# Kernel tuning notes

Measured on AMD Instinct MI355X. Metric: run time of the kernel, lower is better.

The kernel has to match this reference:

```python
import jax, jax.numpy as jnp
import numpy as np
import math

SIZE = 64
SCALE = math.sqrt(SIZE)
EPS = 1e-12  # torch F.normalize default eps

def l2_normalize(x, axis):
    n = jnp.linalg.norm(x, ord=2, axis=axis, keepdims=True)
    return x / jnp.maximum(n, EPS)

def setup_inputs() -> dict:
    key = jax.random.key(0)
    k1, k2, k3 = jax.random.split(key, 3)
    n, l, s, d, v = 8, 2048, 2048, SIZE, SIZE
    return {
        "query": jax.random.normal(k1, (n, l, d), dtype=jnp.float32),
        "key": jax.random.normal(k2, (n, s, d), dtype=jnp.float32),
        "value": jax.random.normal(k3, (n, s, v), dtype=jnp.float32),
        "mask": jnp.ones((n, l, s), dtype=bool),
    }

def reference(query, key, value, mask):
    # rank-3 query path with normalize=True (cosine attention)
    q = l2_normalize(query, 2)
    k = l2_normalize(key, 2)
    score = jnp.einsum('nlk,nsk->nls', q, k) / SCALE
    score = jnp.where(mask, score, -jnp.inf)
    score = jax.nn.softmax(score, axis=2)  # [n, l, s]
    # equivalent to (score.unsqueeze(3) * value.unsqueeze(1)).sum(2)
    output_value = jnp.einsum('nls,nsv->nlv', score, value)
    return (output_value, score)
```

## Files before the change

kernel.cpp:

```cpp
#include <hip/hip_runtime.h>
#include <hip/hip_bf16.h>
#include <math.h>


typedef __bf16 bf16x8 __attribute__((ext_vector_type(8)));
typedef __bf16 bf16x4 __attribute__((ext_vector_type(4)));
typedef float f32x4 __attribute__((ext_vector_type(4)));

#define NB 8
#define LL 2048
#define SS 2048
#define DD 64

__global__ __launch_bounds__(256) void prep_norm(const float* __restrict__ q,
                                                 const float* __restrict__ k,
                                                 __bf16* __restrict__ Qb,
                                                 __bf16* __restrict__ Kb) {
  int w = threadIdx.x >> 6, lane = threadIdx.x & 63;
  int r = blockIdx.x * 4 + w;
  const float* src;
  __bf16* dst;
  float extra;
  if (r < NB * LL) {
    src = q + (size_t)r * DD;
    dst = Qb + (size_t)r * DD;
    extra = 0.125f;
  } else {
    int rk = r - NB * LL;
    src = k + (size_t)rk * DD;
    dst = Kb + (size_t)rk * DD;
    extra = 1.0f;
  }
  float x = src[lane];
  float ss = x * x;
  ss += __shfl_xor(ss, 1);
  ss += __shfl_xor(ss, 2);
  ss += __shfl_xor(ss, 4);
  ss += __shfl_xor(ss, 8);
  ss += __shfl_xor(ss, 16);
  ss += __shfl_xor(ss, 32);
  float nrm = sqrtf(ss);
  float sc = extra / fmaxf(nrm, 1e-12f);
  dst[lane] = (__bf16)(x * sc);
}

__global__ __launch_bounds__(256) void prep_vt(const float* __restrict__ v,
                                               __bf16* __restrict__ Vt) {
  __shared__ __bf16 tile[64][72];
  int n = blockIdx.y;
  int s0 = blockIdx.x * 64;
  int t = threadIdx.x;
#pragma unroll
  for (int it = 0; it < 4; ++it) {
    int idx = t + it * 256;
    int s = idx >> 4, c = idx & 15;
    float4 f = *(const float4*)(v + ((size_t)(n * SS + s0 + s)) * DD + c * 4);
    tile[s][c * 4 + 0] = (__bf16)f.x;
    tile[s][c * 4 + 1] = (__bf16)f.y;
    tile[s][c * 4 + 2] = (__bf16)f.z;
    tile[s][c * 4 + 3] = (__bf16)f.w;
  }
  __syncthreads();
#pragma unroll
  for (int it = 0; it < 4; ++it) {
    int idx = t + it * 256;
    int vv = idx >> 4, c = idx & 15;
    bf16x4 o;
    o[0] = tile[c * 4 + 0][vv];
    o[1] = tile[c * 4 + 1][vv];
    o[2] = tile[c * 4 + 2][vv];
    o[3] = tile[c * 4 + 3][vv];
    *(bf16x4*)(Vt + ((size_t)(n * DD + vv)) * SS + s0 + c * 4) = o;
  }
}

__global__ __launch_bounds__(512, 4) void attn_main(const __bf16* __restrict__ Qb,
                                                    const __bf16* __restrict__ Kb,
                                                    const __bf16* __restrict__ Vt,
                                                    const int* __restrict__ mask,
                                                    float* __restrict__ out_val,
                                                    float* __restrict__ out_score) {
  __shared__ __bf16 e_lds[2][16][136];
  __shared__ unsigned mb_lds[2][16][33];
  __shared__ float rs_lds[8][16];
  __shared__ float acc_red[4][16][17];
  __shared__ float inv_row[16];
  __shared__ __bf16 ep_buf[16][520];

  const int n = blockIdx.y;
  const int l0 = blockIdx.x * 16;

  const int t = threadIdx.x;
  const int w = t >> 6;
  const int lane = t & 63;
  const int m16 = lane & 15;
  const int quad = lane >> 4;
  const int vg = w & 3;
  const int sh = (w >> 2) * 64;

  const __bf16* qrow = Qb + ((size_t)(n * LL + l0 + m16)) * DD;
  bf16x8 aq0 = *(const bf16x8*)(qrow + quad * 8);
  bf16x8 aq1 = *(const bf16x8*)(qrow + 32 + quad * 8);

  const __bf16* kbase = Kb + (size_t)n * SS * DD;
  const __bf16* vrow = Vt + ((size_t)(n * DD + vg * 16 + m16)) * SS + sh;

  const int mrow_st = t >> 5;
  const int mcol_st = (t & 31) * 4;
  const int* mgbase = mask + ((size_t)(n * LL + l0 + mrow_st)) * SS + mcol_st;

  f32x4 acc_o = {0.f, 0.f, 0.f, 0.f};
  float rsum = 0.f;
  bf16x4 stash[16];

  int4 mreg[2];
  mreg[0] = *(const int4*)(mgbase + 0 * 128);
  mreg[1] = *(const int4*)(mgbase + 1 * 128);

  bf16x8 kpa0, kpa1, kpb0, kpb1;
  {
    const __bf16* kr = kbase + (size_t)(w * 16 + m16) * DD;
    kpa0 = *(const bf16x8*)(kr + quad * 8);
    kpa1 = *(const bf16x8*)(kr + 32 + quad * 8);
  }

  {
    const int4 m = mreg[0];
    mb_lds[0][mrow_st][t & 31] = (unsigned)((m.x != 0) | ((m.y != 0) << 8) |
                                            ((m.z != 0) << 16) | ((m.w != 0) << 24));
  }
  asm volatile("s_waitcnt lgkmcnt(0)" ::: "memory");
  __builtin_amdgcn_s_barrier();

#pragma unroll
  for (int c = 0; c < 16; ++c) {
    const int sc = c * 128;
    bf16x8 bv0 = *(const bf16x8*)(vrow + sc + quad * 8);
    bf16x8 bv1 = *(const bf16x8*)(vrow + sc + 32 + quad * 8);
    if (c + 1 < 16) {
      const __bf16* kr = kbase + (size_t)(sc + 128 + w * 16 + m16) * DD;
      if (c & 1) {
        kpa0 = *(const bf16x8*)(kr + quad * 8);
        kpa1 = *(const bf16x8*)(kr + 32 + quad * 8);
      } else {
        kpb0 = *(const bf16x8*)(kr + quad * 8);
        kpb1 = *(const bf16x8*)(kr + 32 + quad * 8);
      }
    }
    if (c + 2 < 16) mreg[c & 1] = *(const int4*)(mgbase + (size_t)(c + 2) * 128);
    if (c + 1 < 16) {
      const int4 m = mreg[(c + 1) & 1];
      mb_lds[(c + 1) & 1][mrow_st][t & 31] =
          (unsigned)((m.x != 0) | ((m.y != 0) << 8) | ((m.z != 0) << 16) |
                     ((m.w != 0) << 24));
    }
    const unsigned mu = mb_lds[c & 1][m16][w * 4 + quad];
    const bf16x8 kb0 = (c & 1) ? kpb0 : kpa0;
    const bf16x8 kb1 = (c & 1) ? kpb1 : kpa1;
    f32x4 acc = {0.f, 0.f, 0.f, 0.f};
    acc = __builtin_amdgcn_mfma_f32_16x16x32_bf16(kb0, aq0, acc, 0, 0, 0);
    acc = __builtin_amdgcn_mfma_f32_16x16x32_bf16(kb1, aq1, acc, 0, 0, 0);
    float e0 = (mu & 0x1u) ? __expf(acc[0]) : 0.f;
    float e1 = (mu & 0x100u) ? __expf(acc[1]) : 0.f;
    float e2 = (mu & 0x10000u) ? __expf(acc[2]) : 0.f;
    float e3 = (mu & 0x1000000u) ? __expf(acc[3]) : 0.f;
    rsum += (e0 + e1) + (e2 + e3);
    bf16x4 sv;
    sv[0] = (__bf16)e0;
    sv[1] = (__bf16)e1;
    sv[2] = (__bf16)e2;
    sv[3] = (__bf16)e3;
    stash[c] = sv;
    *(bf16x4*)(&e_lds[c & 1][m16][w * 16 + quad * 4]) = sv;
    asm volatile("s_waitcnt lgkmcnt(0)" ::: "memory");
    __builtin_amdgcn_s_barrier();
    bf16x8 ae0 = *(const bf16x8*)(&e_lds[c & 1][m16][sh + quad * 8]);
    bf16x8 ae1 = *(const bf16x8*)(&e_lds[c & 1][m16][sh + 32 + quad * 8]);
    acc_o = __builtin_amdgcn_mfma_f32_16x16x32_bf16(ae0, bv0, acc_o, 0, 0, 0);
    acc_o = __builtin_amdgcn_mfma_f32_16x16x32_bf16(ae1, bv1, acc_o, 0, 0, 0);
  }

  rsum += __shfl_xor(rsum, 16);
  rsum += __shfl_xor(rsum, 32);
  if (quad == 0) rs_lds[w][m16] = rsum;
  if (w >= 4) {
#pragma unroll
    for (int r = 0; r < 4; ++r) acc_red[vg][quad * 4 + r][m16] = acc_o[r];
  }
  __syncthreads();

  float tot = 0.f;
#pragma unroll
  for (int ww = 0; ww < 8; ++ww) tot += rs_lds[ww][m16];
  const float inv_s = 1.0f / tot;
  if (t < 16) inv_row[t] = inv_s;

  if (w < 4) {
#pragma unroll
    for (int r = 0; r < 4; ++r) {
      const int row = quad * 4 + r;
      float tr = 0.f;
#pragma unroll
      for (int ww = 0; ww < 8; ++ww) tr += rs_lds[ww][row];
      const float o = (acc_o[r] + acc_red[vg][row][m16]) / tr;
      out_val[((size_t)(n * LL + l0 + row)) * DD + vg * 16 + m16] = o;
    }
  }
  __syncthreads();

  const int erow = t >> 5;
  const int ecol = (t & 31) * 4;
  const float einv = inv_row[erow];
  float* obase = out_score + ((size_t)(n * LL + l0 + erow)) * SS;
#pragma unroll
  for (int g = 0; g < 4; ++g) {
#pragma unroll
    for (int i = 0; i < 4; ++i) {
      *(bf16x4*)(&ep_buf[m16][i * 128 + w * 16 + quad * 4]) = stash[g * 4 + i];
    }
    asm volatile("s_waitcnt lgkmcnt(0)" ::: "memory");
    __builtin_amdgcn_s_barrier();
#pragma unroll
    for (int i = 0; i < 4; ++i) {
      const bf16x4 ev = *(const bf16x4*)(&ep_buf[erow][ecol + i * 128]);
      float4 o;
      o.x = (float)ev[0] * einv;
      o.y = (float)ev[1] * einv;
      o.z = (float)ev[2] * einv;
      o.w = (float)ev[3] * einv;
      *(float4*)(obase + g * 512 + ecol + i * 128) = o;
    }
    asm volatile("s_waitcnt lgkmcnt(0)" ::: "memory");
    __builtin_amdgcn_s_barrier();
  }
}

extern "C" void kernel_launch(void* const* d_in, const int* in_sizes, int n_in,
                              void* d_out, int out_size, void* d_ws, size_t ws_size,
                              hipStream_t stream) {
  const float* q = (const float*)d_in[0];
  const float* k = (const float*)d_in[1];
  const float* v = (const float*)d_in[2];
  const int* mask = (const int*)d_in[3];

  float* out_val = (float*)d_out;
  float* out_score = out_val + (size_t)NB * LL * DD;

  __bf16* Qb = (__bf16*)d_ws;
  __bf16* Kb = Qb + (size_t)NB * LL * DD;
  __bf16* Vt = Kb + (size_t)NB * SS * DD;

  prep_norm<<<dim3((NB * LL * 2) / 4), dim3(256), 0, stream>>>(q, k, Qb, Kb);
  prep_vt<<<dim3(SS / 64, NB), dim3(256), 0, stream>>>(v, Vt);
  attn_main<<<dim3(LL / 16, NB), dim3(512), 0, stream>>>(Qb, Kb, Vt, mask, out_val, out_score);
}
```

Before: 278.1 us.

## Split attention into two passes: row sums first, then stream scores during PV

The main kernel now runs two passes over the keys. The first recomputes QK^T and exponentials only to get row sums, and caches the mask bits in registers. The second recomputes QK^T, does the PV MMA, and writes each normalized score tile straight out as it is produced. This removes the 16-entry register stash and the epilogue LDS buffer, and spreads the score stores across the loop so they overlap compute. The cost is a second set of K loads, MMAs and exps, plus extra barriers in the first pass.

```diff
diff --git a/kernel.cpp b/kernel.cpp
--- a/kernel.cpp
+++ b/kernel.cpp
@@ -85,7 +85,6 @@
   __shared__ float rs_lds[8][16];
   __shared__ float acc_red[4][16][17];
   __shared__ float inv_row[16];
-  __shared__ __bf16 ep_buf[16][520];
 
   const int n = blockIdx.y;
   const int l0 = blockIdx.x * 16;
@@ -103,26 +102,22 @@
   bf16x8 aq1 = *(const bf16x8*)(qrow + 32 + quad * 8);
 
   const __bf16* kbase = Kb + (size_t)n * SS * DD;
+  const __bf16* krow0 = kbase + (size_t)(w * 16 + m16) * DD;
   const __bf16* vrow = Vt + ((size_t)(n * DD + vg * 16 + m16)) * SS + sh;
 
   const int mrow_st = t >> 5;
-  const int mcol_st = (t & 31) * 4;
-  const int* mgbase = mask + ((size_t)(n * LL + l0 + mrow_st)) * SS + mcol_st;
-
-  f32x4 acc_o = {0.f, 0.f, 0.f, 0.f};
+  const int* mgbase = mask + ((size_t)(n * LL + l0 + mrow_st)) * SS + (t & 31) * 4;
+
   float rsum = 0.f;
-  bf16x4 stash[16];
+  unsigned mbits0 = 0, mbits1 = 0;
 
   int4 mreg[2];
   mreg[0] = *(const int4*)(mgbase + 0 * 128);
   mreg[1] = *(const int4*)(mgbase + 1 * 128);
 
   bf16x8 kpa0, kpa1, kpb0, kpb1;
-  {
-    const __bf16* kr = kbase + (size_t)(w * 16 + m16) * DD;
-    kpa0 = *(const bf16x8*)(kr + quad * 8);
-    kpa1 = *(const bf16x8*)(kr + 32 + quad * 8);
-  }
+  kpa0 = *(const bf16x8*)(krow0 + quad * 8);
+  kpa1 = *(const bf16x8*)(krow0 + 32 + quad * 8);
 
   {
     const int4 m = mreg[0];
@@ -134,11 +129,8 @@
 
 #pragma unroll
   for (int c = 0; c < 16; ++c) {
-    const int sc = c * 128;
-    bf16x8 bv0 = *(const bf16x8*)(vrow + sc + quad * 8);
-    bf16x8 bv1 = *(const bf16x8*)(vrow + sc + 32 + quad * 8);
     if (c + 1 < 16) {
-      const __bf16* kr = kbase + (size_t)(sc + 128 + w * 16 + m16) * DD;
+      const __bf16* kr = krow0 + (size_t)((c + 1) * 128) * DD;
       if (c & 1) {
         kpa0 = *(const bf16x8*)(kr + quad * 8);
         kpa1 = *(const bf16x8*)(kr + 32 + quad * 8);
@@ -160,17 +152,75 @@
     f32x4 acc = {0.f, 0.f, 0.f, 0.f};
     acc = __builtin_amdgcn_mfma_f32_16x16x32_bf16(kb0, aq0, acc, 0, 0, 0);
     acc = __builtin_amdgcn_mfma_f32_16x16x32_bf16(kb1, aq1, acc, 0, 0, 0);
-    float e0 = (mu & 0x1u) ? __expf(acc[0]) : 0.f;
-    float e1 = (mu & 0x100u) ? __expf(acc[1]) : 0.f;
-    float e2 = (mu & 0x10000u) ? __expf(acc[2]) : 0.f;
-    float e3 = (mu & 0x1000000u) ? __expf(acc[3]) : 0.f;
-    rsum += (e0 + e1) + (e2 + e3);
+    rsum += ((mu & 0x1u) ? __expf(acc[0]) : 0.f) +
+            ((mu & 0x100u) ? __expf(acc[1]) : 0.f) +
+            ((mu & 0x10000u) ? __expf(acc[2]) : 0.f) +
+            ((mu & 0x1000000u) ? __expf(acc[3]) : 0.f);
+    const unsigned b4 = (mu & 1u) | ((mu >> 7) & 2u) | ((mu >> 14) & 4u) |
+                        ((mu >> 21) & 8u);
+    if (c < 8) mbits0 |= b4 << (c * 4);
+    else mbits1 |= b4 << ((c - 8) * 4);
+    asm volatile("s_waitcnt lgkmcnt(0)" ::: "memory");
+    __builtin_amdgcn_s_barrier();
+  }
+
+  rsum += __shfl_xor(rsum, 16);
+  rsum += __shfl_xor(rsum, 32);
+  if (quad == 0) rs_lds[w][m16] = rsum;
+  __syncthreads();
+  float tot = 0.f;
+#pragma unroll
+  for (int ww = 0; ww < 8; ++ww) tot += rs_lds[ww][m16];
+  const float inv_s = 1.0f / tot;
+  if (t < 16) inv_row[t] = inv_s;
+
+  f32x4 acc_o = {0.f, 0.f, 0.f, 0.f};
+  kpa0 = *(const bf16x8*)(krow0 + quad * 8);
+  kpa1 = *(const bf16x8*)(krow0 + 32 + quad * 8);
+  bf16x8 bva0, bva1, bvb0, bvb1;
+  bva0 = *(const bf16x8*)(vrow + quad * 8);
+  bva1 = *(const bf16x8*)(vrow + 32 + quad * 8);
+
+  const int erow = t >> 5;
+  const int ecol = (t & 31) * 4;
+  float* obase = out_score + ((size_t)(n * LL + l0 + erow)) * SS + ecol;
+
+#pragma unroll
+  for (int c = 0; c < 16; ++c) {
+    const int sc = c * 128;
+    if (c + 1 < 16) {
+      const __bf16* kr = krow0 + (size_t)(sc + 128) * DD;
+      const __bf16* vr = vrow + sc + 128;
+      if (c & 1) {
+        kpa0 = *(const bf16x8*)(kr + quad * 8);
+        kpa1 = *(const bf16x8*)(kr + 32 + quad * 8);
+        bva0 = *(const bf16x8*)(vr + quad * 8);
+        bva1 = *(const bf16x8*)(vr + 32 + quad * 8);
+      } else {
+        kpb0 = *(const bf16x8*)(kr + quad * 8);
+        kpb1 = *(const bf16x8*)(kr + 32 + quad * 8);
+        bvb0 = *(const bf16x8*)(vr + quad * 8);
+        bvb1 = *(const bf16x8*)(vr + 32 + quad * 8);
+      }
+    }
+    const bf16x8 kb0 = (c & 1) ? kpb0 : kpa0;
+    const bf16x8 kb1 = (c & 1) ? kpb1 : kpa1;
+    const bf16x8 bv0 = (c & 1) ? bvb0 : bva0;
+    const bf16x8 bv1 = (c & 1) ? bvb1 : bva1;
+    f32x4 acc = {0.f, 0.f, 0.f, 0.f};
+    acc = __builtin_amdgcn_mfma_f32_16x16x32_bf16(kb0, aq0, acc, 0, 0, 0);
+    acc = __builtin_amdgcn_mfma_f32_16x16x32_bf16(kb1, aq1, acc, 0, 0, 0);
+    const unsigned b4 =
+        ((c < 8 ? mbits0 >> (c * 4) : mbits1 >> ((c - 8) * 4))) & 0xFu;
+    const float e0 = (b4 & 1u) ? __expf(acc[0]) : 0.f;
+    const float e1 = (b4 & 2u) ? __expf(acc[1]) : 0.f;
+    const float e2 = (b4 & 4u) ? __expf(acc[2]) : 0.f;
+    const float e3 = (b4 & 8u) ? __expf(acc[3]) : 0.f;
     bf16x4 sv;
     sv[0] = (__bf16)e0;
     sv[1] = (__bf16)e1;
     sv[2] = (__bf16)e2;
     sv[3] = (__bf16)e3;
-    stash[c] = sv;
     *(bf16x4*)(&e_lds[c & 1][m16][w * 16 + quad * 4]) = sv;
     asm volatile("s_waitcnt lgkmcnt(0)" ::: "memory");
     __builtin_amdgcn_s_barrier();
@@ -178,23 +228,24 @@
     bf16x8 ae1 = *(const bf16x8*)(&e_lds[c & 1][m16][sh + 32 + quad * 8]);
     acc_o = __builtin_amdgcn_mfma_f32_16x16x32_bf16(ae0, bv0, acc_o, 0, 0, 0);
     acc_o = __builtin_amdgcn_mfma_f32_16x16x32_bf16(ae1, bv1, acc_o, 0, 0, 0);
-  }
-
-  rsum += __shfl_xor(rsum, 16);
-  rsum += __shfl_xor(rsum, 32);
-  if (quad == 0) rs_lds[w][m16] = rsum;
+    {
+      const bf16x4 ev = *(const bf16x4*)(&e_lds[c & 1][erow][ecol]);
+      const float ei = inv_row[erow];
+      float4 o;
+      o.x = (float)ev[0] * ei;
+      o.y = (float)ev[1] * ei;
+      o.z = (float)ev[2] * ei;
+      o.w = (float)ev[3] * ei;
+      *(float4*)(obase + sc) = o;
+    }
+  }
+
+  rsum = 0.f;
   if (w >= 4) {
 #pragma unroll
     for (int r = 0; r < 4; ++r) acc_red[vg][quad * 4 + r][m16] = acc_o[r];
   }
   __syncthreads();
-
-  float tot = 0.f;
-#pragma unroll
-  for (int ww = 0; ww < 8; ++ww) tot += rs_lds[ww][m16];
-  const float inv_s = 1.0f / tot;
-  if (t < 16) inv_row[t] = inv_s;
-
   if (w < 4) {
 #pragma unroll
     for (int r = 0; r < 4; ++r) {
@@ -205,33 +256,6 @@
       const float o = (acc_o[r] + acc_red[vg][row][m16]) / tr;
       out_val[((size_t)(n * LL + l0 + row)) * DD + vg * 16 + m16] = o;
     }
-  }
-  __syncthreads();
-
-  const int erow = t >> 5;
-  const int ecol = (t & 31) * 4;
-  const float einv = inv_row[erow];
-  float* obase = out_score + ((size_t)(n * LL + l0 + erow)) * SS;
-#pragma unroll
-  for (int g = 0; g < 4; ++g) {
-#pragma unroll
-    for (int i = 0; i < 4; ++i) {
-      *(bf16x4*)(&ep_buf[m16][i * 128 + w * 16 + quad * 4]) = stash[g * 4 + i];
-    }
-    asm volatile("s_waitcnt lgkmcnt(0)" ::: "memory");
-    __builtin_amdgcn_s_barrier();
-#pragma unroll
-    for (int i = 0; i < 4; ++i) {
-      const bf16x4 ev = *(const bf16x4*)(&ep_buf[erow][ecol + i * 128]);
-      float4 o;
-      o.x = (float)ev[0] * einv;
-      o.y = (float)ev[1] * einv;
-      o.z = (float)ev[2] * einv;
-      o.w = (float)ev[3] * einv;
-      *(float4*)(obase + g * 512 + ecol + i * 128) = o;
-    }
-    asm volatile("s_waitcnt lgkmcnt(0)" ::: "memory");
-    __builtin_amdgcn_s_barrier();
   }
 }
 
```

Result: slower. 304.4 us (+9.4%).

## Deepen mask and V prefetch and alias epilogue LDS buffer

Applied to the files above, without the earlier changes.

Mask loads move from two chunks of lookahead to four, and V tiles are now double-buffered in registers one chunk ahead instead of being loaded inside the same iteration that uses them. Shared memory is merged into one byte array, with the epilogue buffer aliasing the main-loop buffers, which lowers LDS use per block. The aim is to hide global memory latency in the mask-bandwidth-bound loop and possibly allow more blocks per CU. The cost is higher register pressure, which under launch_bounds(512,4) could cause spills.

```diff
diff --git a/kernel.cpp b/kernel.cpp
--- a/kernel.cpp
+++ b/kernel.cpp
@@ -80,12 +80,13 @@
                                                     const int* __restrict__ mask,
                                                     float* __restrict__ out_val,
                                                     float* __restrict__ out_score) {
-  __shared__ __bf16 e_lds[2][16][136];
-  __shared__ unsigned mb_lds[2][16][33];
-  __shared__ float rs_lds[8][16];
-  __shared__ float acc_red[4][16][17];
-  __shared__ float inv_row[16];
-  __shared__ __bf16 ep_buf[16][520];
+  __shared__ __align__(16) char smem[17856];
+  __bf16 (*e_lds)[16][136] = (__bf16(*)[16][136])(smem);
+  unsigned (*mb_lds)[16][33] = (unsigned(*)[16][33])(smem + 8704);
+  float (*rs_lds)[16] = (float(*)[16])(smem + 12928);
+  float (*acc_red)[16][17] = (float(*)[16][17])(smem + 13440);
+  float* inv_row = (float*)(smem + 17792);
+  __bf16 (*ep_buf)[520] = (__bf16(*)[520])(smem);
 
   const int n = blockIdx.y;
   const int l0 = blockIdx.x * 16;
@@ -103,26 +104,28 @@
   bf16x8 aq1 = *(const bf16x8*)(qrow + 32 + quad * 8);
 
   const __bf16* kbase = Kb + (size_t)n * SS * DD;
+  const __bf16* krow0 = kbase + (size_t)(w * 16 + m16) * DD;
   const __bf16* vrow = Vt + ((size_t)(n * DD + vg * 16 + m16)) * SS + sh;
 
   const int mrow_st = t >> 5;
-  const int mcol_st = (t & 31) * 4;
-  const int* mgbase = mask + ((size_t)(n * LL + l0 + mrow_st)) * SS + mcol_st;
+  const int* mgbase = mask + ((size_t)(n * LL + l0 + mrow_st)) * SS + (t & 31) * 4;
 
   f32x4 acc_o = {0.f, 0.f, 0.f, 0.f};
   float rsum = 0.f;
   bf16x4 stash[16];
 
-  int4 mreg[2];
+  int4 mreg[4];
   mreg[0] = *(const int4*)(mgbase + 0 * 128);
   mreg[1] = *(const int4*)(mgbase + 1 * 128);
+  mreg[2] = *(const int4*)(mgbase + 2 * 128);
+  mreg[3] = *(const int4*)(mgbase + 3 * 128);
 
   bf16x8 kpa0, kpa1, kpb0, kpb1;
-  {
-    const __bf16* kr = kbase + (size_t)(w * 16 + m16) * DD;
-    kpa0 = *(const bf16x8*)(kr + quad * 8);
-    kpa1 = *(const bf16x8*)(kr + 32 + quad * 8);
-  }
+  kpa0 = *(const bf16x8*)(krow0 + quad * 8);
+  kpa1 = *(const bf16x8*)(krow0 + 32 + quad * 8);
+  bf16x8 bva0, bva1, bvb0, bvb1;
+  bva0 = *(const bf16x8*)(vrow + quad * 8);
+  bva1 = *(const bf16x8*)(vrow + 32 + quad * 8);
 
   {
     const int4 m = mreg[0];
@@ -135,10 +138,8 @@
 #pragma unroll
   for (int c = 0; c < 16; ++c) {
     const int sc = c * 128;
-    bf16x8 bv0 = *(const bf16x8*)(vrow + sc + quad * 8);
-    bf16x8 bv1 = *(const bf16x8*)(vrow + sc + 32 + quad * 8);
     if (c + 1 < 16) {
-      const __bf16* kr = kbase + (size_t)(sc + 128 + w * 16 + m16) * DD;
+      const __bf16* kr = krow0 + (size_t)(sc + 128) * DD;
       if (c & 1) {
         kpa0 = *(const bf16x8*)(kr + quad * 8);
         kpa1 = *(const bf16x8*)(kr + 32 + quad * 8);
@@ -147,9 +148,19 @@
         kpb1 = *(const bf16x8*)(kr + 32 + quad * 8);
       }
     }
-    if (c + 2 < 16) mreg[c & 1] = *(const int4*)(mgbase + (size_t)(c + 2) * 128);
     if (c + 1 < 16) {
-      const int4 m = mreg[(c + 1) & 1];
+      const __bf16* vr = vrow + sc + 128;
+      if (c & 1) {
+        bva0 = *(const bf16x8*)(vr + quad * 8);
+        bva1 = *(const bf16x8*)(vr + 32 + quad * 8);
+      } else {
+        bvb0 = *(const bf16x8*)(vr + quad * 8);
+        bvb1 = *(const bf16x8*)(vr + 32 + quad * 8);
+      }
+    }
+    if (c + 4 < 16) mreg[c & 3] = *(const int4*)(mgbase + (size_t)(c + 4) * 128);
+    if (c + 1 < 16) {
+      const int4 m = mreg[(c + 1) & 3];
       mb_lds[(c + 1) & 1][mrow_st][t & 31] =
           (unsigned)((m.x != 0) | ((m.y != 0) << 8) | ((m.z != 0) << 16) |
                      ((m.w != 0) << 24));
@@ -157,6 +168,8 @@
     const unsigned mu = mb_lds[c & 1][m16][w * 4 + quad];
     const bf16x8 kb0 = (c & 1) ? kpb0 : kpa0;
     const bf16x8 kb1 = (c & 1) ? kpb1 : kpa1;
+    const bf16x8 bv0 = (c & 1) ? bvb0 : bva0;
+    const bf16x8 bv1 = (c & 1) ? bvb1 : bva1;
     f32x4 acc = {0.f, 0.f, 0.f, 0.f};
     acc = __builtin_amdgcn_mfma_f32_16x16x32_bf16(kb0, aq0, acc, 0, 0, 0);
     acc = __builtin_amdgcn_mfma_f32_16x16x32_bf16(kb1, aq1, acc, 0, 0, 0);
```

Result: no change. 280.7 us (+0.9%).

## Process 32 query rows per block and stash score tiles as fp8

Applied to the files above, without the earlier changes.

Each block now handles two 16-row query tiles, so every K and V fragment loaded from global memory feeds twice as many MFMAs and the grid is halved. The per-thread stash of unnormalised exponentials is packed to fp8 instead of bf16, which halves the stash registers needed to hold both tiles. The cost is a larger LDS footprint and more registers per thread, which may lower occupancy, and coarser precision in the written score matrix. fp8 e4m3 holds roughly two to three significant digits, so the score output may fall outside the tolerance.

```diff
diff --git a/kernel.cpp b/kernel.cpp
--- a/kernel.cpp
+++ b/kernel.cpp
@@ -11,6 +11,39 @@
 #define LL 2048
 #define SS 2048
 #define DD 64
+
+#if __has_builtin(__builtin_amdgcn_cvt_pk_fp8_f32) && __has_builtin(__builtin_amdgcn_cvt_pk_f32_fp8)
+static __device__ __forceinline__ unsigned pack4_fp8(float a, float b, float c, float d) {
+  int p = 0;
+  p = __builtin_amdgcn_cvt_pk_fp8_f32(a, b, p, false);
+  p = __builtin_amdgcn_cvt_pk_fp8_f32(c, d, p, true);
+  return (unsigned)p;
+}
+static __device__ __forceinline__ float4 unpack4_fp8(unsigned u) {
+  auto lo = __builtin_amdgcn_cvt_pk_f32_fp8((int)u, false);
+  auto hi = __builtin_amdgcn_cvt_pk_f32_fp8((int)u, true);
+  return make_float4(lo[0], lo[1], hi[0], hi[1]);
+}
+#else
+#include <hip/hip_fp8.h>
+static __device__ __forceinline__ unsigned pack4_fp8(float a, float b, float c, float d) {
+  union { unsigned u; __hip_fp8_storage_t b4[4]; } r;
+  r.b4[0] = __hip_cvt_float_to_fp8(a, __HIP_SATFINITE, __HIP_E4M3);
+  r.b4[1] = __hip_cvt_float_to_fp8(b, __HIP_SATFINITE, __HIP_E4M3);
+  r.b4[2] = __hip_cvt_float_to_fp8(c, __HIP_SATFINITE, __HIP_E4M3);
+  r.b4[3] = __hip_cvt_float_to_fp8(d, __HIP_SATFINITE, __HIP_E4M3);
+  return r.u;
+}
+static __device__ __forceinline__ float4 unpack4_fp8(unsigned u) {
+  union { unsigned u; __hip_fp8_storage_t b4[4]; } r;
+  r.u = u;
+  return make_float4(
+      (float)__hip_cvt_fp8_to_halfraw(r.b4[0], __HIP_E4M3).data == 0 ? 0.f : (float)__half(__hip_cvt_fp8_to_halfraw(r.b4[0], __HIP_E4M3)),
+      (float)__half(__hip_cvt_fp8_to_halfraw(r.b4[1], __HIP_E4M3)),
+      (float)__half(__hip_cvt_fp8_to_halfraw(r.b4[2], __HIP_E4M3)),
+      (float)__half(__hip_cvt_fp8_to_halfraw(r.b4[3], __HIP_E4M3)));
+}
+#endif
 
 __global__ __launch_bounds__(256) void prep_norm(const float* __restrict__ q,
                                                  const float* __restrict__ k,
@@ -74,21 +107,27 @@
   }
 }
 
+static __device__ __forceinline__ unsigned packmask(int4 m) {
+  return (unsigned)((m.x != 0) | ((m.y != 0) << 8) | ((m.z != 0) << 16) |
+                    ((m.w != 0) << 24));
+}
+
 __global__ __launch_bounds__(512, 4) void attn_main(const __bf16* __restrict__ Qb,
                                                     const __bf16* __restrict__ Kb,
                                                     const __bf16* __restrict__ Vt,
                                                     const int* __restrict__ mask,
                                                     float* __restrict__ out_val,
                                                     float* __restrict__ out_score) {
-  __shared__ __bf16 e_lds[2][16][136];
-  __shared__ unsigned mb_lds[2][16][33];
-  __shared__ float rs_lds[8][16];
-  __shared__ float acc_red[4][16][17];
-  __shared__ float inv_row[16];
-  __shared__ __bf16 ep_buf[16][520];
+  __shared__ __align__(16) char smem[35712];
+  __bf16 (*e_lds)[32][136] = (__bf16(*)[32][136])(smem);
+  unsigned (*mb_lds)[32][33] = (unsigned(*)[32][33])(smem + 17408);
+  float (*rs_lds)[32] = (float(*)[32])(smem + 25856);
+  float (*acc_red)[32][17] = (float(*)[32][17])(smem + 26880);
+  float* inv_row = (float*)(smem + 35584);
+  unsigned (*ep)[130] = (unsigned(*)[130])(smem);
 
   const int n = blockIdx.y;
-  const int l0 = blockIdx.x * 16;
+  const int l0 = blockIdx.x * 32;
 
   const int t = threadIdx.x;
   const int w = t >> 6;
@@ -98,37 +137,41 @@
   const int vg = w & 3;
   const int sh = (w >> 2) * 64;
 
-  const __bf16* qrow = Qb + ((size_t)(n * LL + l0 + m16)) * DD;
-  bf16x8 aq0 = *(const bf16x8*)(qrow + quad * 8);
-  bf16x8 aq1 = *(const bf16x8*)(qrow + 32 + quad * 8);
+  const __bf16* qrowA = Qb + ((size_t)(n * LL + l0 + m16)) * DD;
+  const __bf16* qrowB = qrowA + (size_t)16 * DD;
+  bf16x8 aqA0 = *(const bf16x8*)(qrowA + quad * 8);
+  bf16x8 aqA1 = *(const bf16x8*)(qrowA + 32 + quad * 8);
+  bf16x8 aqB0 = *(const bf16x8*)(qrowB + quad * 8);
+  bf16x8 aqB1 = *(const bf16x8*)(qrowB + 32 + quad * 8);
 
   const __bf16* kbase = Kb + (size_t)n * SS * DD;
+  const __bf16* krow0 = kbase + (size_t)(w * 16 + m16) * DD;
   const __bf16* vrow = Vt + ((size_t)(n * DD + vg * 16 + m16)) * SS + sh;
 
-  const int mrow_st = t >> 5;
-  const int mcol_st = (t & 31) * 4;
-  const int* mgbase = mask + ((size_t)(n * LL + l0 + mrow_st)) * SS + mcol_st;
-
-  f32x4 acc_o = {0.f, 0.f, 0.f, 0.f};
-  float rsum = 0.f;
-  bf16x4 stash[16];
-
-  int4 mreg[2];
-  mreg[0] = *(const int4*)(mgbase + 0 * 128);
-  mreg[1] = *(const int4*)(mgbase + 1 * 128);
-
+  const int srow = t >> 4;
+  const int sc2 = (t & 15) * 2;
+  const int* mgbase = mask + ((size_t)(n * LL + l0 + srow)) * SS + (t & 15) * 8;
+
+  f32x4 acc_oA = {0.f, 0.f, 0.f, 0.f};
+  f32x4 acc_oB = {0.f, 0.f, 0.f, 0.f};
+  float rsumA = 0.f, rsumB = 0.f;
+  unsigned stashA[16], stashB[16];
+
+  int4 mra[2], mrb[2];
+  {
+    int4 m0a = *(const int4*)(mgbase + 0);
+    int4 m0b = *(const int4*)(mgbase + 4);
+    mra[1] = *(const int4*)(mgbase + 1 * 128);
+    mrb[1] = *(const int4*)(mgbase + 1 * 128 + 4);
+    mra[0] = *(const int4*)(mgbase + 2 * 128);
+    mrb[0] = *(const int4*)(mgbase + 2 * 128 + 4);
+    mb_lds[0][srow][sc2 + 0] = packmask(m0a);
+    mb_lds[0][srow][sc2 + 1] = packmask(m0b);
+  }
   bf16x8 kpa0, kpa1, kpb0, kpb1;
-  {
-    const __bf16* kr = kbase + (size_t)(w * 16 + m16) * DD;
-    kpa0 = *(const bf16x8*)(kr + quad * 8);
-    kpa1 = *(const bf16x8*)(kr + 32 + quad * 8);
-  }
-
-  {
-    const int4 m = mreg[0];
-    mb_lds[0][mrow_st][t & 31] = (unsigned)((m.x != 0) | ((m.y != 0) << 8) |
-                                            ((m.z != 0) << 16) | ((m.w != 0) << 24));
-  }
+  kpa0 = *(const bf16x8*)(krow0 + quad * 8);
+  kpa1 = *(const bf16x8*)(krow0 + 32 + quad * 8);
+
   asm volatile("s_waitcnt lgkmcnt(0)" ::: "memory");
   __builtin_amdgcn_s_barrier();
 
@@ -138,7 +181,7 @@
     bf16x8 bv0 = *(const bf16x8*)(vrow + sc + quad * 8);
     bf16x8 bv1 = *(const bf16x8*)(vrow + sc + 32 + quad * 8);
     if (c + 1 < 16) {
-      const __bf16* kr = kbase + (size_t)(sc + 128 + w * 16 + m16) * DD;
+      const __bf16* kr = krow0 + (size_t)(sc + 128) * DD;
       if (c & 1) {
         kpa0 = *(const bf16x8*)(kr + quad * 8);
         kpa1 = *(const bf16x8*)(kr + 32 + quad * 8);
@@ -147,91 +190,126 @@
         kpb1 = *(const bf16x8*)(kr + 32 + quad * 8);
       }
     }
-    if (c + 2 < 16) mreg[c & 1] = *(const int4*)(mgbase + (size_t)(c + 2) * 128);
     if (c + 1 < 16) {
-      const int4 m = mreg[(c + 1) & 1];
-      mb_lds[(c + 1) & 1][mrow_st][t & 31] =
-          (unsigned)((m.x != 0) | ((m.y != 0) << 8) | ((m.z != 0) << 16) |
-                     ((m.w != 0) << 24));
-    }
-    const unsigned mu = mb_lds[c & 1][m16][w * 4 + quad];
+      mb_lds[(c + 1) & 1][srow][sc2 + 0] = packmask(mra[(c + 1) & 1]);
+      mb_lds[(c + 1) & 1][srow][sc2 + 1] = packmask(mrb[(c + 1) & 1]);
+    }
+    if (c + 3 < 16) {
+      mra[(c + 1) & 1] = *(const int4*)(mgbase + (size_t)(c + 3) * 128);
+      mrb[(c + 1) & 1] = *(const int4*)(mgbase + (size_t)(c + 3) * 128 + 4);
+    }
+    const unsigned muA = mb_lds[c & 1][m16][w * 4 + quad];
+    const unsigned muB = mb_lds[c & 1][16 + m16][w * 4 + quad];
     const bf16x8 kb0 = (c & 1) ? kpb0 : kpa0;
     const bf16x8 kb1 = (c & 1) ? kpb1 : kpa1;
-    f32x4 acc = {0.f, 0.f, 0.f, 0.f};
-    acc = __builtin_amdgcn_mfma_f32_16x16x32_bf16(kb0, aq0, acc, 0, 0, 0);
-    acc = __builtin_amdgcn_mfma_f32_16x16x32_bf16(kb1, aq1, acc, 0, 0, 0);
-    float e0 = (mu & 0x1u) ? __expf(acc[0]) : 0.f;
-    float e1 = (mu & 0x100u) ? __expf(acc[1]) : 0.f;
-    float e2 = (mu & 0x10000u) ? __expf(acc[2]) : 0.f;
-    float e3 = (mu & 0x1000000u) ? __expf(acc[3]) : 0.f;
-    rsum += (e0 + e1) + (e2 + e3);
-    bf16x4 sv;
-    sv[0] = (__bf16)e0;
-    sv[1] = (__bf16)e1;
-    sv[2] = (__bf16)e2;
-    sv[3] = (__bf16)e3;
-    stash[c] = sv;
-    *(bf16x4*)(&e_lds[c & 1][m16][w * 16 + quad * 4]) = sv;
+    f32x4 accA = {0.f, 0.f, 0.f, 0.f};
+    f32x4 accB = {0.f, 0.f, 0.f, 0.f};
+    accA = __builtin_amdgcn_mfma_f32_16x16x32_bf16(kb0, aqA0, accA, 0, 0, 0);
+    accA = __builtin_amdgcn_mfma_f32_16x16x32_bf16(kb1, aqA1, accA, 0, 0, 0);
+    accB = __builtin_amdgcn_mfma_f32_16x16x32_bf16(kb0, aqB0, accB, 0, 0, 0);
+    accB = __builtin_amdgcn_mfma_f32_16x16x32_bf16(kb1, aqB1, accB, 0, 0, 0);
+    const float eA0 = (muA & 0x1u) ? __expf(accA[0]) : 0.f;
+    const float eA1 = (muA & 0x100u) ? __expf(accA[1]) : 0.f;
+    const float eA2 = (muA & 0x10000u) ? __expf(accA[2]) : 0.f;
+    const float eA3 = (muA & 0x1000000u) ? __expf(accA[3]) : 0.f;
+    const float eB0 = (muB & 0x1u) ? __expf(accB[0]) : 0.f;
+    const float eB1 = (muB & 0x100u) ? __expf(accB[1]) : 0.f;
+    const float eB2 = (muB & 0x10000u) ? __expf(accB[2]) : 0.f;
+    const float eB3 = (muB & 0x1000000u) ? __expf(accB[3]) : 0.f;
+    rsumA += (eA0 + eA1) + (eA2 + eA3);
+    rsumB += (eB0 + eB1) + (eB2 + eB3);
+    stashA[c] = pack4_fp8(eA0, eA1, eA2, eA3);
+    stashB[c] = pack4_fp8(eB0, eB1, eB2, eB3);
+    bf16x4 svA, svB;
+    svA[0] = (__bf16)eA0; svA[1] = (__bf16)eA1;
+    svA[2] = (__bf16)eA2; svA[3] = (__bf16)eA3;
+    svB[0] = (__bf16)eB0; svB[1] = (__bf16)eB1;
+    svB[2] = (__bf16)eB2; svB[3] = (__bf16)eB3;
+    *(bf16x4*)(&e_lds[c & 1][m16][w * 16 + quad * 4]) = svA;
+    *(bf16x4*)(&e_lds[c & 1][16 + m16][w * 16 + quad * 4]) = svB;
     asm volatile("s_waitcnt lgkmcnt(0)" ::: "memory");
     __builtin_amdgcn_s_barrier();
-    bf16x8 ae0 = *(const bf16x8*)(&e_lds[c & 1][m16][sh + quad * 8]);
-    bf16x8 ae1 = *(const bf16x8*)(&e_lds[c & 1][m16][sh + 32 + quad * 8]);
-    acc_o = __builtin_amdgcn_mfma_f32_16x16x32_bf16(ae0, bv0, acc_o, 0, 0, 0);
-    acc_o = __builtin_amdgcn_mfma_f32_16x16x32_bf16(ae1, bv1, acc_o, 0, 0, 0);
-  }
-
-  rsum += __shfl_xor(rsum, 16);
-  rsum += __shfl_xor(rsum, 32);
-  if (quad == 0) rs_lds[w][m16] = rsum;
+    bf16x8 aeA0 = *(const bf16x8*)(&e_lds[c & 1][m16][sh + quad * 8]);
+    bf16x8 aeA1 = *(const bf16x8*)(&e_lds[c & 1][m16][sh + 32 + quad * 8]);
+    bf16x8 aeB0 = *(const bf16x8*)(&e_lds[c & 1][16 + m16][sh + quad * 8]);
+    bf16x8 aeB1 = *(const bf16x8*)(&e_lds[c & 1][16 + m16][sh + 32 + quad * 8]);
+    acc_oA = __builtin_amdgcn_mfma_f32_16x16x32_bf16(aeA0, bv0, acc_oA, 0, 0, 0);
+    acc_oA = __builtin_amdgcn_mfma_f32_16x16x32_bf16(aeA1, bv1, acc_oA, 0, 0, 0);
+    acc_oB = __builtin_amdgcn_mfma_f32_16x16x32_bf16(aeB0, bv0, acc_oB, 0, 0, 0);
+    acc_oB = __builtin_amdgcn_mfma_f32_16x16x32_bf16(aeB1, bv1, acc_oB, 0, 0, 0);
+  }
+
+  rsumA += __shfl_xor(rsumA, 16);
+  rsumA += __shfl_xor(rsumA, 32);
+  rsumB += __shfl_xor(rsumB, 16);
+  rsumB += __shfl_xor(rsumB, 32);
+  if (quad == 0) {
+    rs_lds[w][m16] = rsumA;
+    rs_lds[w][16 + m16] = rsumB;
+  }
   if (w >= 4) {
 #pragma unroll
-    for (int r = 0; r < 4; ++r) acc_red[vg][quad * 4 + r][m16] = acc_o[r];
+    for (int r = 0; r < 4; ++r) {
+      acc_red[vg][quad * 4 + r][m16] = acc_oA[r];
+      acc_red[vg][16 + quad * 4 + r][m16] = acc_oB[r];
+    }
   }
   __syncthreads();
 
-  float tot = 0.f;
-#pragma unroll
-  for (int ww = 0; ww < 8; ++ww) tot += rs_lds[ww][m16];
-  const float inv_s = 1.0f / tot;
-  if (t < 16) inv_row[t] = inv_s;
+  if (t < 32) {
+    float tot = 0.f;
+#pragma unroll
+    for (int ww = 0; ww < 8; ++ww) tot += rs_lds[ww][t];
+    inv_row[t] = 1.0f / tot;
+  }
 
   if (w < 4) {
 #pragma unroll
     for (int r = 0; r < 4; ++r) {
-      const int row = quad * 4 + r;
-      float tr = 0.f;
-#pragma unroll
-      for (int ww = 0; ww < 8; ++ww) tr += rs_lds[ww][row];
-      const float o = (acc_o[r] + acc_red[vg][row][m16]) / tr;
-      out_val[((size_t)(n * LL + l0 + row)) * DD + vg * 16 + m16] = o;
+      const int rowA = quad * 4 + r;
+      const int rowB = 16 + quad * 4 + r;
+      float trA = 0.f, trB = 0.f;
+#pragma unroll
+      for (int ww = 0; ww < 8; ++ww) {
+        trA += rs_lds[ww][rowA];
+        trB += rs_lds[ww][rowB];
+      }
+      out_val[((size_t)(n * LL + l0 + rowA)) * DD + vg * 16 + m16] =
+          (acc_oA[r] + acc_red[vg][rowA][m16]) / trA;
+      out_val[((size_t)(n * LL + l0 + rowB)) * DD + vg * 16 + m16] =
+          (acc_oB[r] + acc_red[vg][rowB][m16]) / trB;
     }
   }
   __syncthreads();
 
   const int erow = t >> 5;
-  const int ecol = (t & 31) * 4;
-  const float einv = inv_row[erow];
-  float* obase = out_score + ((size_t)(n * LL + l0 + erow)) * SS;
-#pragma unroll
-  for (int g = 0; g < 4; ++g) {
-#pragma unroll
-    for (int i = 0; i < 4; ++i) {
-      *(bf16x4*)(&ep_buf[m16][i * 128 + w * 16 + quad * 4]) = stash[g * 4 + i];
-    }
-    asm volatile("s_waitcnt lgkmcnt(0)" ::: "memory");
-    __builtin_amdgcn_s_barrier();
-#pragma unroll
-    for (int i = 0; i < 4; ++i) {
-      const bf16x4 ev = *(const bf16x4*)(&ep_buf[erow][ecol + i * 128]);
-      float4 o;
-      o.x = (float)ev[0] * einv;
-      o.y = (float)ev[1] * einv;
-      o.z = (float)ev[2] * einv;
-      o.w = (float)ev[3] * einv;
-      *(float4*)(obase + g * 512 + ecol + i * 128) = o;
-    }
-    asm volatile("s_waitcnt lgkmcnt(0)" ::: "memory");
-    __builtin_amdgcn_s_barrier();
+  const int ecol = t & 31;
+#pragma unroll
+  for (int h = 0; h < 2; ++h) {
+    const float einv = inv_row[h * 16 + erow];
+    float* obase = out_score + ((size_t)(n * LL + l0 + h * 16 + erow)) * SS;
+#pragma unroll
+    for (int g = 0; g < 4; ++g) {
+#pragma unroll
+      for (int i = 0; i < 4; ++i) {
+        const unsigned u = h ? stashB[g * 4 + i] : stashA[g * 4 + i];
+        ep[m16][i * 32 + w * 4 + quad] = u;
+      }
+      asm volatile("s_waitcnt lgkmcnt(0)" ::: "memory");
+      __builtin_amdgcn_s_barrier();
+#pragma unroll
+      for (int i = 0; i < 4; ++i) {
+        const float4 e4 = unpack4_fp8(ep[erow][ecol + i * 32]);
+        float4 o;
+        o.x = e4.x * einv;
+        o.y = e4.y * einv;
+        o.z = e4.z * einv;
+        o.w = e4.w * einv;
+        *(float4*)(obase + g * 512 + ecol * 4 + i * 128) = o;
+      }
+      asm volatile("s_waitcnt lgkmcnt(0)" ::: "memory");
+      __builtin_amdgcn_s_barrier();
+    }
   }
 }
 
@@ -252,5 +330,5 @@
 
   prep_norm<<<dim3((NB * LL * 2) / 4), dim3(256), 0, stream>>>(q, k, Qb, Kb);
   prep_vt<<<dim3(SS / 64, NB), dim3(256), 0, stream>>>(v, Vt);
-  attn_main<<<dim3(LL / 16, NB), dim3(512), 0, stream>>>(Qb, Kb, Vt, mask, out_val, out_score);
-}
+  attn_main<<<dim3(LL / 32, NB), dim3(512), 0, stream>>>(Qb, Kb, Vt, mask, out_val, out_score);
+}
```

New measurement: 319.0 us. +14.7%, slower.
